# Optimization experiments

Hardware: AMD Instinct MI355X
Metric: run time of the kernel (lower is better)

## Reference

```python
import jax, jax.numpy as jnp
import numpy as np

N_HEAD = 16
HEAD_DIM = 64  # n_embd // n_head = 1024 // 16


def setup_inputs() -> dict:
    key = jax.random.key(0)
    k1, k2, k3 = jax.random.split(key, 3)
    B, T, C = 4, 2048, 1024
    x = jax.random.normal(k1, (B, T, C), dtype=jnp.float32)
    # torch Linear weight is (out, in); we store transposed (in, out) for x @ W
    w_qkv = jax.random.normal(k2, (C, 3 * C), dtype=jnp.float32) * (1.0 / np.sqrt(C))
    w_out = jax.random.normal(k3, (C, C), dtype=jnp.float32) * (1.0 / np.sqrt(C))
    return {"x": x, "w_qkv": w_qkv, "w_out": w_out}


def reference(x, w_qkv, w_out):
    B, T, C = x.shape
    scale = 1.0 / np.sqrt(HEAD_DIM).astype(np.float32)
    qkv = x @ w_qkv                                   # [B, T, 3C]
    q, k, v = jnp.split(qkv, 3, axis=2)
    def heads(t):  # [B, T, C] -> [B, H, T, Dh]
        return t.reshape(B, T, N_HEAD, HEAD_DIM).transpose(0, 2, 1, 3)
    q, k, v = heads(q), heads(k), heads(v)
    att = jnp.einsum('bhqd,bhkd->bhqk', q, k) * scale  # [B, H, T, T]
    causal = jnp.tril(jnp.ones((T, T), dtype=bool))
    att = jnp.where(causal[None, None], att, jnp.float32(-jnp.inf))
    att = jax.nn.softmax(att, axis=-1)
    y = jnp.einsum('bhqk,bhkd->bhqd', att, v)          # [B, H, T, Dh]
    y = y.transpose(0, 2, 1, 3).reshape(B, T, C)
    return y @ w_out
```

## Files before the change

### kernel.cpp

```cpp
#include <hip/hip_runtime.h>
#include <hip/hip_bf16.h>

#define B_ 4
#define T_ 2048
#define C_ 1024
#define H_ 16
#define D_ 64

typedef __bf16 bf16x8 __attribute__((ext_vector_type(8)));
typedef float f32x4 __attribute__((ext_vector_type(4)));
typedef float f32x16 __attribute__((ext_vector_type(16)));

__device__ __forceinline__ unsigned short f2bs(float f) {
    __hip_bfloat16 h = __float2bfloat16(f);
    return *reinterpret_cast<unsigned short*>(&h);
}

__device__ __forceinline__ float fexp2(float x) {
    float r;
    asm("v_exp_f32 %0, %1" : "=v"(r) : "v"(x));
    return r;
}

__device__ __forceinline__ unsigned cvtpk(float a, float b) {
    unsigned r;
    asm("v_cvt_pk_bf16_f32 %0, %1, %2" : "=v"(r) : "v"(a), "v"(b));
    return r;
}

__device__ __forceinline__ void plane32swap(unsigned& a, unsigned& b, int hi) {
#if __has_builtin(__builtin_amdgcn_permlane32_swap)
    typedef int i32x2 __attribute__((ext_vector_type(2)));
    i32x2 r = __builtin_amdgcn_permlane32_swap((int)a, (int)b, false, false);
    a = (unsigned)r.x; b = (unsigned)r.y;
#else
    unsigned v = hi ? a : b;
    unsigned e = __shfl_xor(v, 32);
    unsigned na = hi ? e : a;
    unsigned nb = hi ? b : e;
    a = na; b = nb;
#endif
}

__device__ __forceinline__ int swz(int row, int col) {
    return (row * 64 + col) ^ ((row & 7) << 3);
}

__device__ __forceinline__ void gload16(const void* g, void* l) {
    auto gp = (const __attribute__((address_space(1))) void*)(g);
    auto lp = (__attribute__((address_space(3))) void*)(uintptr_t)(l);
    __builtin_amdgcn_global_load_lds(gp, lp, 16, 0, 0);
}

__device__ __forceinline__ void phase_barrier() {
    __builtin_amdgcn_sched_barrier(0x77);
    __builtin_amdgcn_s_barrier();
}

__global__ __launch_bounds__(256)
void cvt_f32_to_bf16(const float* __restrict__ in, unsigned short* __restrict__ out, int n4) {
    int i = blockIdx.x * 256 + threadIdx.x;
    if (i >= n4) return;
    float4 v = ((const float4*)in)[i];
    union { unsigned short h[4]; uint2 u; } pk;
    pk.h[0] = f2bs(v.x); pk.h[1] = f2bs(v.y);
    pk.h[2] = f2bs(v.z); pk.h[3] = f2bs(v.w);
    ((uint2*)out)[i] = pk.u;
}

__global__ __launch_bounds__(256)
void transpose_weights(const float* __restrict__ in1, unsigned short* __restrict__ out1,
                       const float* __restrict__ in2, unsigned short* __restrict__ out2) {
    __shared__ float tile[64][65];
    const int tx = threadIdx.x & 63;
    const int ty = threadIdx.x >> 6;
    const bool second = blockIdx.x >= 48;
    const float* in = second ? in2 : in1;
    unsigned short* out = second ? out2 : out1;
    const int C = second ? 1024 : 3072;
    const int R = 1024;
    const int c0 = (second ? (blockIdx.x - 48) : blockIdx.x) * 64;
    const int r0 = blockIdx.y * 64;
    #pragma unroll
    for (int i = 0; i < 16; ++i) {
        int r = ty * 16 + i;
        tile[r][tx] = in[(size_t)(r0 + r) * C + c0 + tx];
    }
    __syncthreads();
    #pragma unroll
    for (int i = 0; i < 16; ++i) {
        int r = ty * 16 + i;
        out[(size_t)(c0 + r) * R + r0 + tx] = f2bs(tile[tx][r]);
    }
}

template<int MODE, int K>
__global__ __launch_bounds__(512, 2)
void gemm256(const unsigned short* __restrict__ A,
             const unsigned short* __restrict__ Bt,
             float* __restrict__ Out, int N_out,
             unsigned short* __restrict__ Qb,
             unsigned short* __restrict__ Kb,
             unsigned short* __restrict__ Vt) {
    __shared__ alignas(16) unsigned short L[2][4][128 * 64];
    const int tid = threadIdx.x;
    const int l = tid & 63;
    const int c16 = l & 15, lq = l >> 4;
    const int wv = tid >> 6;
    const int wm = wv >> 2;
    const int wn = wv & 3;
    const int m0 = blockIdx.x * 256, n0 = blockIdx.y * 256;
    constexpr int NT = K / 64;

    f32x4 acc[8][4];
    #pragma unroll
    for (int i = 0; i < 8; ++i)
        #pragma unroll
        for (int j = 0; j < 4; ++j)
            acc[i][j] = f32x4{0.f, 0.f, 0.f, 0.f};

    const int srow = tid >> 3;
    const int scs  = tid & 7;
    const int ldsbase = (tid & ~63) * 8;

    auto stage = [&](const unsigned short* M, int row0, int k0, unsigned short* dst) {
        #pragma unroll
        for (int r = 0; r < 2; ++r) {
            int row = r * 64 + srow;
            int csw = 8 * (scs ^ (row & 7));
            gload16(&M[(size_t)(row0 + row) * K + k0 + csw], &dst[r * 4096 + ldsbase]);
        }
    };

    stage(A,  m0,       0, L[0][0]);
    stage(A,  m0 + 128, 0, L[0][1]);
    stage(Bt, n0,       0, L[0][2]);
    stage(Bt, n0 + 128, 0, L[0][3]);
    if (NT > 1) stage(A, m0, 64, L[1][0]);

    bf16x8 af[4][2], bf[2][2], bg[2][2];
    const int brow0 = (wn & 1) * 64;

    for (int t = 0; t < NT; ++t) {
        const unsigned short* ap = L[t & 1][wm];
        const unsigned short* bp = L[t & 1][2 + (wn >> 1)];
        const int kn = (t + 1) * 64;

        if (t == NT - 1) asm volatile("s_waitcnt vmcnt(0)" ::: "memory");
        else             asm volatile("s_waitcnt vmcnt(2)" ::: "memory");
        #pragma unroll
        for (int mi = 0; mi < 4; ++mi)
            #pragma unroll
            for (int kk = 0; kk < 2; ++kk)
                af[mi][kk] = *(const bf16x8*)&ap[swz(mi * 16 + c16, kk * 32 + lq * 8)];
        #pragma unroll
        for (int ni = 0; ni < 2; ++ni)
            #pragma unroll
            for (int kk = 0; kk < 2; ++kk)
                bf[ni][kk] = *(const bf16x8*)&bp[swz(brow0 + ni * 16 + c16, kk * 32 + lq * 8)];
        if (t + 1 < NT) stage(A, m0 + 128, kn, L[(t + 1) & 1][1]);
        phase_barrier();
        __builtin_amdgcn_s_setprio(1);
        #pragma unroll
        for (int mi = 0; mi < 4; ++mi)
            #pragma unroll
            for (int ni = 0; ni < 2; ++ni)
                #pragma unroll
                for (int kk = 0; kk < 2; ++kk)
                    acc[mi][ni] = __builtin_amdgcn_mfma_f32_16x16x32_bf16(
                        af[mi][kk], bf[ni][kk], acc[mi][ni], 0, 0, 0);
        __builtin_amdgcn_s_setprio(0);
        phase_barrier();

        #pragma unroll
        for (int ni = 0; ni < 2; ++ni)
            #pragma unroll
            for (int kk = 0; kk < 2; ++kk)
                bg[ni][kk] = *(const bf16x8*)&bp[swz(brow0 + (ni + 2) * 16 + c16, kk * 32 + lq * 8)];
        if (t + 1 < NT) stage(Bt, n0, kn, L[(t + 1) & 1][2]);
        phase_barrier();
        __builtin_amdgcn_s_setprio(1);
        #pragma unroll
        for (int mi = 0; mi < 4; ++mi)
            #pragma unroll
            for (int ni = 0; ni < 2; ++ni)
                #pragma unroll
                for (int kk = 0; kk < 2; ++kk)
                    acc[mi][ni + 2] = __builtin_amdgcn_mfma_f32_16x16x32_bf16(
                        af[mi][kk], bg[ni][kk], acc[mi][ni + 2], 0, 0, 0);
        __builtin_amdgcn_s_setprio(0);
        phase_barrier();

        #pragma unroll
        for (int mi = 0; mi < 4; ++mi)
            #pragma unroll
            for (int kk = 0; kk < 2; ++kk)
                af[mi][kk] = *(const bf16x8*)&ap[swz((mi + 4) * 16 + c16, kk * 32 + lq * 8)];
        if (t + 1 < NT) stage(Bt, n0 + 128, kn, L[(t + 1) & 1][3]);
        phase_barrier();
        __builtin_amdgcn_s_setprio(1);
        #pragma unroll
        for (int mi = 0; mi < 4; ++mi)
            #pragma unroll
            for (int ni = 0; ni < 2; ++ni)
                #pragma unroll
                for (int kk = 0; kk < 2; ++kk)
                    acc[mi + 4][ni + 2] = __builtin_amdgcn_mfma_f32_16x16x32_bf16(
                        af[mi][kk], bg[ni][kk], acc[mi + 4][ni + 2], 0, 0, 0);
        __builtin_amdgcn_s_setprio(0);
        phase_barrier();

        if (t + 2 < NT) stage(A, m0, (t + 2) * 64, L[t & 1][0]);
        phase_barrier();
        __builtin_amdgcn_s_setprio(1);
        #pragma unroll
        for (int mi = 0; mi < 4; ++mi)
            #pragma unroll
            for (int ni = 0; ni < 2; ++ni)
                #pragma unroll
                for (int kk = 0; kk < 2; ++kk)
                    acc[mi + 4][ni] = __builtin_amdgcn_mfma_f32_16x16x32_bf16(
                        af[mi][kk], bf[ni][kk], acc[mi + 4][ni], 0, 0, 0);
        __builtin_amdgcn_s_setprio(0);
        phase_barrier();
    }

    #pragma unroll
    for (int mi = 0; mi < 8; ++mi) {
        #pragma unroll
        for (int ni = 0; ni < 4; ++ni) {
            #pragma unroll
            for (int r = 0; r < 4; ++r) {
                float v = acc[mi][ni][r];
                int row = m0 + wm * 128 + mi * 16 + lq * 4 + r;
                int col = n0 + wn * 64 + ni * 16 + c16;
                if (MODE == 1) {
                    Out[(size_t)row * N_out + col] = v;
                } else {
                    int which = col >> 10;
                    int c = col & 1023;
                    int h = c >> 6, d = c & 63;
                    int b = row >> 11, t = row & 2047;
                    int bh = b * H_ + h;
                    if (which == 0)
                        Qb[((size_t)(bh * T_ + t)) * D_ + d] = f2bs(v * 0.1803368801111204f);
                    else if (which == 1)
                        Kb[((size_t)(bh * T_ + t)) * D_ + d] = f2bs(v);
                    else
                        Vt[((size_t)(bh * D_ + d)) * T_ + t] = f2bs(v);
                }
            }
        }
    }
}

template<int MODE>
__global__ __launch_bounds__(256)
void gemm_bt(const unsigned short* __restrict__ A,
             const unsigned short* __restrict__ Bt,
             float* __restrict__ Out, int N_out,
             unsigned short* __restrict__ Qb,
             unsigned short* __restrict__ Kb,
             unsigned short* __restrict__ Vt,
             int K) {
    __shared__ alignas(16) unsigned short As[2][128 * 64];
    __shared__ alignas(16) unsigned short Bs[2][128 * 64];
    const int tid = threadIdx.x;
    const int l = tid & 63;
    const int c16 = l & 15, lq = l >> 4;
    const int wv = tid >> 6;
    const int wrow = wv >> 1, wcol = wv & 1;
    const int m0 = blockIdx.x * 128, n0 = blockIdx.y * 128;

    f32x4 acc[4][4];
    #pragma unroll
    for (int i = 0; i < 4; ++i)
        #pragma unroll
        for (int j = 0; j < 4; ++j)
            acc[i][j] = f32x4{0.f, 0.f, 0.f, 0.f};

    const int srow = tid >> 3;
    const int scs  = tid & 7;
    const int ldsbase = (tid & ~63) * 8;

    auto stage = [&](int k0, int buf) {
        #pragma unroll
        for (int p = 0; p < 4; ++p) {
            int row = p * 32 + srow;
            int csw = 8 * (scs ^ (row & 7));
            gload16(&A[(size_t)(m0 + row) * K + k0 + csw], &As[buf][p * 2048 + ldsbase]);
            gload16(&Bt[(size_t)(n0 + row) * K + k0 + csw], &Bs[buf][p * 2048 + ldsbase]);
        }
    };

    stage(0, 0);
    const int NK = K >> 6;
    for (int i = 0; i < NK; ++i) {
        __syncthreads();
        if (i + 1 < NK) stage((i + 1) << 6, (i + 1) & 1);
        const unsigned short* Al = As[i & 1];
        const unsigned short* Bl = Bs[i & 1];
        #pragma unroll
        for (int kk = 0; kk < 64; kk += 32) {
            bf16x8 af[4], bfv[4];
            int koff = kk + lq * 8;
            #pragma unroll
            for (int t = 0; t < 4; ++t) {
                af[t]  = *(const bf16x8*)&Al[swz(wrow * 64 + t * 16 + c16, koff)];
                bfv[t] = *(const bf16x8*)&Bl[swz(wcol * 64 + t * 16 + c16, koff)];
            }
            #pragma unroll
            for (int mi = 0; mi < 4; ++mi)
                #pragma unroll
                for (int ni = 0; ni < 4; ++ni)
                    acc[mi][ni] = __builtin_amdgcn_mfma_f32_16x16x32_bf16(
                        af[mi], bfv[ni], acc[mi][ni], 0, 0, 0);
        }
    }

    #pragma unroll
    for (int mi = 0; mi < 4; ++mi) {
        #pragma unroll
        for (int ni = 0; ni < 4; ++ni) {
            #pragma unroll
            for (int r = 0; r < 4; ++r) {
                float v = acc[mi][ni][r];
                int row = m0 + wrow * 64 + mi * 16 + lq * 4 + r;
                int col = n0 + wcol * 64 + ni * 16 + c16;
                if (MODE == 1) {
                    Out[(size_t)row * N_out + col] = v;
                } else {
                    int which = col >> 10;
                    int c = col & 1023;
                    int h = c >> 6, d = c & 63;
                    int b = row >> 11, t = row & 2047;
                    int bh = b * H_ + h;
                    if (which == 0)
                        Qb[((size_t)(bh * T_ + t)) * D_ + d] = f2bs(v * 0.1803368801111204f);
                    else if (which == 1)
                        Kb[((size_t)(bh * T_ + t)) * D_ + d] = f2bs(v);
                    else
                        Vt[((size_t)(bh * D_ + d)) * T_ + t] = f2bs(v);
                }
            }
        }
    }
}

__global__ __launch_bounds__(256, 2)
void attn_fwd(const unsigned short* __restrict__ Qb,
              const unsigned short* __restrict__ Kb,
              const unsigned short* __restrict__ Vt,
              unsigned short* __restrict__ Y) {
    __shared__ alignas(16) unsigned short Ks[2][64 * 64];
    __shared__ alignas(16) unsigned short Vs[2][64 * 64];
    const int tid = threadIdx.x;
    const int wv = tid >> 6;
    const int l = tid & 63;
    const int r32 = l & 31;
    const int hi = l >> 5;
    const int hi8 = hi * 8;
    const int bh = blockIdx.x & 63;
    const int qp = blockIdx.x >> 6;
    const unsigned short* Kp = Kb + (size_t)bh * T_ * D_;
    const unsigned short* Vp = Vt + (size_t)bh * D_ * T_;
    const unsigned short* Qbase = Qb + (size_t)bh * T_ * D_;
    const int b = bh >> 4, h = bh & 15;
    const int srow = tid >> 3;
    const int scs  = tid & 7;
    const int scol_sw = 8 * (scs ^ (srow & 7));
    const int wbase = wv * 512;

    #pragma unroll
    for (int half = 0; half < 2; ++half) {
        const int qc = (half == 0) ? qp : 15 - qp;
        const int q0w = qc * 128 + wv * 32;
        const int nt = 2 * qc + 2;
        const int qg = q0w + r32;

        bf16x8 qf[4];
        #pragma unroll
        for (int ds = 0; ds < 4; ++ds)
            qf[ds] = *(const bf16x8*)&Qbase[(size_t)qg * 64 + ds * 16 + hi8];

        f32x16 o[2];
        #pragma unroll
        for (int e = 0; e < 16; ++e) { o[0][e] = 0.f; o[1][e] = 0.f; }
        float lsum = 0.f;

        __syncthreads();
        gload16(&Kp[(size_t)srow * 64 + scol_sw],        &Ks[0][wbase]);
        gload16(&Kp[(size_t)(srow + 32) * 64 + scol_sw], &Ks[0][2048 + wbase]);
        gload16(&Vp[(size_t)srow * T_ + scol_sw],        &Vs[0][wbase]);
        gload16(&Vp[(size_t)(srow + 32) * T_ + scol_sw], &Vs[0][2048 + wbase]);

        for (int it = 0; it < nt; ++it) {
            const int kb = it * 64;
            __syncthreads();
            if (it + 1 < nt) {
                const int kn = kb + 64;
                unsigned short* Kd = Ks[(it + 1) & 1];
                unsigned short* Vd = Vs[(it + 1) & 1];
                gload16(&Kp[(size_t)(kn + srow) * 64 + scol_sw],        &Kd[wbase]);
                gload16(&Kp[(size_t)(kn + srow + 32) * 64 + scol_sw],   &Kd[2048 + wbase]);
                gload16(&Vp[(size_t)srow * T_ + kn + scol_sw],          &Vd[wbase]);
                gload16(&Vp[(size_t)(srow + 32) * T_ + kn + scol_sw],   &Vd[2048 + wbase]);
            }
            if (kb > q0w + 31) continue;
            const unsigned short* Kl = Ks[it & 1];
            const unsigned short* Vl = Vs[it & 1];

            f32x16 s[2];
            #pragma unroll
            for (int e = 0; e < 16; ++e) { s[0][e] = 0.f; s[1][e] = 0.f; }
            __builtin_amdgcn_s_setprio(1);
            #pragma unroll
            for (int kt = 0; kt < 2; ++kt)
                #pragma unroll
                for (int ds = 0; ds < 4; ++ds) {
                    bf16x8 af = *(const bf16x8*)&Kl[swz(32 * kt + r32, ds * 16 + hi8)];
                    s[kt] = __builtin_amdgcn_mfma_f32_32x32x16_bf16(af, qf[ds], s[kt], 0, 0, 0);
                }
            __builtin_amdgcn_s_setprio(0);
            if (kb + 63 > q0w) {
                #pragma unroll
                for (int kt = 0; kt < 2; ++kt)
                    #pragma unroll
                    for (int m = 0; m < 4; ++m)
                        #pragma unroll
                        for (int r = 0; r < 4; ++r)
                            if (kb + 32 * kt + 8 * m + r + 4 * hi > qg)
                                s[kt][4 * m + r] = -1e30f;
            }
            float rs0 = 0.f, rs1 = 0.f, rs2 = 0.f, rs3 = 0.f;
            #pragma unroll
            for (int kt = 0; kt < 2; ++kt)
                #pragma unroll
                for (int m = 0; m < 4; ++m) {
                    float p0 = fexp2(s[kt][4 * m + 0]);
                    float p1 = fexp2(s[kt][4 * m + 1]);
                    float p2 = fexp2(s[kt][4 * m + 2]);
                    float p3 = fexp2(s[kt][4 * m + 3]);
                    s[kt][4 * m + 0] = p0; s[kt][4 * m + 1] = p1;
                    s[kt][4 * m + 2] = p2; s[kt][4 * m + 3] = p3;
                    rs0 += p0; rs1 += p1; rs2 += p2; rs3 += p3;
                }
            lsum += (rs0 + rs1) + (rs2 + rs3);
            bf16x8 pb[4];
            #pragma unroll
            for (int ks = 0; ks < 4; ++ks) {
                const int kt = ks >> 1;
                const int m0 = (ks & 1) * 2;
                unsigned a0 = cvtpk(s[kt][4 * m0 + 0], s[kt][4 * m0 + 1]);
                unsigned a1 = cvtpk(s[kt][4 * m0 + 2], s[kt][4 * m0 + 3]);
                unsigned b0 = cvtpk(s[kt][4 * m0 + 4], s[kt][4 * m0 + 5]);
                unsigned b1 = cvtpk(s[kt][4 * m0 + 6], s[kt][4 * m0 + 7]);
                plane32swap(a0, b0, hi);
                plane32swap(a1, b1, hi);
                uint4 u = {a0, a1, b0, b1};
                pb[ks] = *reinterpret_cast<bf16x8*>(&u);
            }
            __builtin_amdgcn_s_setprio(1);
            #pragma unroll
            for (int dt = 0; dt < 2; ++dt)
                #pragma unroll
                for (int ks = 0; ks < 4; ++ks) {
                    bf16x8 va = *(const bf16x8*)&Vl[swz(32 * dt + r32, ks * 16 + hi8)];
                    o[dt] = __builtin_amdgcn_mfma_f32_32x32x16_bf16(va, pb[ks], o[dt], 0, 0, 0);
                }
            __builtin_amdgcn_s_setprio(0);
        }

        float lt = lsum + __shfl_xor(lsum, 32);
        float inv = 1.f / lt;
        #pragma unroll
        for (int dt = 0; dt < 2; ++dt)
            #pragma unroll
            for (int m = 0; m < 4; ++m) {
                uint2 w;
                w.x = cvtpk(o[dt][4 * m + 0] * inv, o[dt][4 * m + 1] * inv);
                w.y = cvtpk(o[dt][4 * m + 2] * inv, o[dt][4 * m + 3] * inv);
                int d = 32 * dt + 8 * m + 4 * hi;
                *(uint2*)&Y[((size_t)(b * T_ + qg)) * C_ + h * D_ + d] = w;
            }
    }
}

extern "C" void kernel_launch(void* const* d_in, const int* in_sizes, int n_in,
                              void* d_out, int out_size, void* d_ws, size_t ws_size,
                              hipStream_t stream) {
    const float* x     = (const float*)d_in[0];
    const float* w_qkv = (const float*)d_in[1];
    const float* w_out = (const float*)d_in[2];
    float* out = (float*)d_out;
    char* ws = (char*)d_ws;

    unsigned short* xb  = (unsigned short*)(ws);
    unsigned short* wqt = (unsigned short*)(ws + (16u << 20));
    unsigned short* wot = (unsigned short*)(ws + (22u << 20));
    unsigned short* Qb  = (unsigned short*)(ws + (24u << 20));
    unsigned short* Kb  = (unsigned short*)(ws + (40u << 20));
    unsigned short* Vt  = (unsigned short*)(ws + (56u << 20));
    unsigned short* Yb  = (unsigned short*)(ws + (72u << 20));

    cvt_f32_to_bf16<<<8192, 256, 0, stream>>>(x, xb, (B_ * T_ * C_) / 4);
    transpose_weights<<<dim3(64, 16), 256, 0, stream>>>(w_qkv, wqt, w_out, wot);
    gemm256<0, 1024><<<dim3(32, 12), 512, 0, stream>>>(xb, wqt, nullptr, 3072, Qb, Kb, Vt);
    attn_fwd<<<512, 256, 0, stream>>>(Qb, Kb, Vt, Yb);
    gemm_bt<1><<<dim3(64, 8), 256, 0, stream>>>(Yb, wot, out, 1024, nullptr, nullptr, nullptr, 1024);
}
```

Measured before the change: 177.6 us.

## Restructure 256x256 GEMM into quadrant-wise wave layout with staggered single-barrier stages

Remaps the 8 waves of the 256x256 GEMM block so each computes a 32x64 piece of each of four 128x128 quadrants, instead of a 128x64 strip. The main loop becomes four segments, each issuing one stage load for the next k-tile, waiting on vmcnt and crossing a single barrier before reusing loaded A/B fragments. This halves the barriers per k-step and interleaves prefetch with MFMA work more evenly. It uses more fragment registers and a looser sched_barrier mask, which risks register pressure or wrong waitcnt ordering.

Result: faster. 169.9 us (-4.3%).

```diff
diff --git a/kernel.cpp b/kernel.cpp
--- a/kernel.cpp
+++ b/kernel.cpp
@@ -52,9 +52,10 @@
     __builtin_amdgcn_global_load_lds(gp, lp, 16, 0, 0);
 }
 
-__device__ __forceinline__ void phase_barrier() {
-    __builtin_amdgcn_sched_barrier(0x77);
+__device__ __forceinline__ void seg_barrier() {
+    __builtin_amdgcn_sched_barrier(0x7);
     __builtin_amdgcn_s_barrier();
+    __builtin_amdgcn_sched_barrier(0x7);
 }
 
 __global__ __launch_bounds__(256)
@@ -107,17 +108,19 @@
     const int l = tid & 63;
     const int c16 = l & 15, lq = l >> 4;
     const int wv = tid >> 6;
-    const int wm = wv >> 2;
-    const int wn = wv & 3;
+    const int rw = wv & 3;
+    const int cw = wv >> 2;
     const int m0 = blockIdx.x * 256, n0 = blockIdx.y * 256;
     constexpr int NT = K / 64;
 
-    f32x4 acc[8][4];
-    #pragma unroll
-    for (int i = 0; i < 8; ++i)
-        #pragma unroll
-        for (int j = 0; j < 4; ++j)
-            acc[i][j] = f32x4{0.f, 0.f, 0.f, 0.f};
+    f32x4 acc[4][2][4];
+    #pragma unroll
+    for (int p = 0; p < 4; ++p)
+        #pragma unroll
+        for (int i = 0; i < 2; ++i)
+            #pragma unroll
+            for (int j = 0; j < 4; ++j)
+                acc[p][i][j] = f32x4{0.f, 0.f, 0.f, 0.f};
 
     const int srow = tid >> 3;
     const int scs  = tid & 7;
@@ -133,121 +136,127 @@
     };
 
     stage(A,  m0,       0, L[0][0]);
+    stage(Bt, n0,       0, L[0][2]);
     stage(A,  m0 + 128, 0, L[0][1]);
-    stage(Bt, n0,       0, L[0][2]);
     stage(Bt, n0 + 128, 0, L[0][3]);
-    if (NT > 1) stage(A, m0, 64, L[1][0]);
-
-    bf16x8 af[4][2], bf[2][2], bg[2][2];
-    const int brow0 = (wn & 1) * 64;
+
+    bf16x8 afA[2][2], afB[2][2], bfA[4][2], bfB[4][2];
 
     for (int t = 0; t < NT; ++t) {
-        const unsigned short* ap = L[t & 1][wm];
-        const unsigned short* bp = L[t & 1][2 + (wn >> 1)];
+        const int cur = t & 1, nb = (t + 1) & 1;
+        const unsigned short* A0 = L[cur][0];
+        const unsigned short* A1 = L[cur][1];
+        const unsigned short* B0 = L[cur][2];
+        const unsigned short* B1 = L[cur][3];
         const int kn = (t + 1) * 64;
-
-        if (t == NT - 1) asm volatile("s_waitcnt vmcnt(0)" ::: "memory");
-        else             asm volatile("s_waitcnt vmcnt(2)" ::: "memory");
-        #pragma unroll
-        for (int mi = 0; mi < 4; ++mi)
+        const bool st = (t + 1) < NT;
+
+        asm volatile("s_waitcnt vmcnt(4)" ::: "memory");
+        if (st) stage(A, m0, kn, L[nb][0]);
+        seg_barrier();
+        #pragma unroll
+        for (int mi = 0; mi < 2; ++mi)
             #pragma unroll
             for (int kk = 0; kk < 2; ++kk)
-                af[mi][kk] = *(const bf16x8*)&ap[swz(mi * 16 + c16, kk * 32 + lq * 8)];
-        #pragma unroll
-        for (int ni = 0; ni < 2; ++ni)
+                afA[mi][kk] = *(const bf16x8*)&A0[swz(rw * 32 + mi * 16 + c16, kk * 32 + lq * 8)];
+        #pragma unroll
+        for (int ni = 0; ni < 4; ++ni)
             #pragma unroll
             for (int kk = 0; kk < 2; ++kk)
-                bf[ni][kk] = *(const bf16x8*)&bp[swz(brow0 + ni * 16 + c16, kk * 32 + lq * 8)];
-        if (t + 1 < NT) stage(A, m0 + 128, kn, L[(t + 1) & 1][1]);
-        phase_barrier();
+                bfA[ni][kk] = *(const bf16x8*)&B0[swz(cw * 64 + ni * 16 + c16, kk * 32 + lq * 8)];
         __builtin_amdgcn_s_setprio(1);
         #pragma unroll
-        for (int mi = 0; mi < 4; ++mi)
-            #pragma unroll
-            for (int ni = 0; ni < 2; ++ni)
+        for (int mi = 0; mi < 2; ++mi)
+            #pragma unroll
+            for (int ni = 0; ni < 4; ++ni)
                 #pragma unroll
                 for (int kk = 0; kk < 2; ++kk)
-                    acc[mi][ni] = __builtin_amdgcn_mfma_f32_16x16x32_bf16(
-                        af[mi][kk], bf[ni][kk], acc[mi][ni], 0, 0, 0);
+                    acc[0][mi][ni] = __builtin_amdgcn_mfma_f32_16x16x32_bf16(
+                        afA[mi][kk], bfA[ni][kk], acc[0][mi][ni], 0, 0, 0);
         __builtin_amdgcn_s_setprio(0);
-        phase_barrier();
-
-        #pragma unroll
-        for (int ni = 0; ni < 2; ++ni)
+
+        if (st) asm volatile("s_waitcnt vmcnt(4)" ::: "memory");
+        else    asm volatile("s_waitcnt vmcnt(2)" ::: "memory");
+        if (st) stage(Bt, n0, kn, L[nb][2]);
+        seg_barrier();
+        #pragma unroll
+        for (int mi = 0; mi < 2; ++mi)
             #pragma unroll
             for (int kk = 0; kk < 2; ++kk)
-                bg[ni][kk] = *(const bf16x8*)&bp[swz(brow0 + (ni + 2) * 16 + c16, kk * 32 + lq * 8)];
-        if (t + 1 < NT) stage(Bt, n0, kn, L[(t + 1) & 1][2]);
-        phase_barrier();
+                afB[mi][kk] = *(const bf16x8*)&A1[swz(rw * 32 + mi * 16 + c16, kk * 32 + lq * 8)];
         __builtin_amdgcn_s_setprio(1);
         #pragma unroll
-        for (int mi = 0; mi < 4; ++mi)
-            #pragma unroll
-            for (int ni = 0; ni < 2; ++ni)
+        for (int mi = 0; mi < 2; ++mi)
+            #pragma unroll
+            for (int ni = 0; ni < 4; ++ni)
                 #pragma unroll
                 for (int kk = 0; kk < 2; ++kk)
-                    acc[mi][ni + 2] = __builtin_amdgcn_mfma_f32_16x16x32_bf16(
-                        af[mi][kk], bg[ni][kk], acc[mi][ni + 2], 0, 0, 0);
+                    acc[1][mi][ni] = __builtin_amdgcn_mfma_f32_16x16x32_bf16(
+                        afB[mi][kk], bfA[ni][kk], acc[1][mi][ni], 0, 0, 0);
         __builtin_amdgcn_s_setprio(0);
-        phase_barrier();
-
-        #pragma unroll
-        for (int mi = 0; mi < 4; ++mi)
+
+        if (st) asm volatile("s_waitcnt vmcnt(4)" ::: "memory");
+        else    asm volatile("s_waitcnt vmcnt(0)" ::: "memory");
+        if (st) stage(A, m0 + 128, kn, L[nb][1]);
+        seg_barrier();
+        #pragma unroll
+        for (int ni = 0; ni < 4; ++ni)
             #pragma unroll
             for (int kk = 0; kk < 2; ++kk)
-                af[mi][kk] = *(const bf16x8*)&ap[swz((mi + 4) * 16 + c16, kk * 32 + lq * 8)];
-        if (t + 1 < NT) stage(Bt, n0 + 128, kn, L[(t + 1) & 1][3]);
-        phase_barrier();
+                bfB[ni][kk] = *(const bf16x8*)&B1[swz(cw * 64 + ni * 16 + c16, kk * 32 + lq * 8)];
         __builtin_amdgcn_s_setprio(1);
         #pragma unroll
-        for (int mi = 0; mi < 4; ++mi)
-            #pragma unroll
-            for (int ni = 0; ni < 2; ++ni)
+        for (int mi = 0; mi < 2; ++mi)
+            #pragma unroll
+            for (int ni = 0; ni < 4; ++ni)
                 #pragma unroll
                 for (int kk = 0; kk < 2; ++kk)
-                    acc[mi + 4][ni + 2] = __builtin_amdgcn_mfma_f32_16x16x32_bf16(
-                        af[mi][kk], bg[ni][kk], acc[mi + 4][ni + 2], 0, 0, 0);
+                    acc[2][mi][ni] = __builtin_amdgcn_mfma_f32_16x16x32_bf16(
+                        afB[mi][kk], bfB[ni][kk], acc[2][mi][ni], 0, 0, 0);
         __builtin_amdgcn_s_setprio(0);
-        phase_barrier();
-
-        if (t + 2 < NT) stage(A, m0, (t + 2) * 64, L[t & 1][0]);
-        phase_barrier();
+
+        if (st) stage(Bt, n0 + 128, kn, L[nb][3]);
+        seg_barrier();
         __builtin_amdgcn_s_setprio(1);
         #pragma unroll
-        for (int mi = 0; mi < 4; ++mi)
-            #pragma unroll
-            for (int ni = 0; ni < 2; ++ni)
+        for (int mi = 0; mi < 2; ++mi)
+            #pragma unroll
+            for (int ni = 0; ni < 4; ++ni)
                 #pragma unroll
                 for (int kk = 0; kk < 2; ++kk)
-                    acc[mi + 4][ni] = __builtin_amdgcn_mfma_f32_16x16x32_bf16(
-                        af[mi][kk], bf[ni][kk], acc[mi + 4][ni], 0, 0, 0);
+                    acc[3][mi][ni] = __builtin_amdgcn_mfma_f32_16x16x32_bf16(
+                        afA[mi][kk], bfB[ni][kk], acc[3][mi][ni], 0, 0, 0);
         __builtin_amdgcn_s_setprio(0);
-        phase_barrier();
-    }
-
-    #pragma unroll
-    for (int mi = 0; mi < 8; ++mi) {
-        #pragma unroll
-        for (int ni = 0; ni < 4; ++ni) {
-            #pragma unroll
-            for (int r = 0; r < 4; ++r) {
-                float v = acc[mi][ni][r];
-                int row = m0 + wm * 128 + mi * 16 + lq * 4 + r;
-                int col = n0 + wn * 64 + ni * 16 + c16;
-                if (MODE == 1) {
-                    Out[(size_t)row * N_out + col] = v;
-                } else {
-                    int which = col >> 10;
-                    int c = col & 1023;
-                    int h = c >> 6, d = c & 63;
-                    int b = row >> 11, t = row & 2047;
-                    int bh = b * H_ + h;
-                    if (which == 0)
-                        Qb[((size_t)(bh * T_ + t)) * D_ + d] = f2bs(v * 0.1803368801111204f);
-                    else if (which == 1)
-                        Kb[((size_t)(bh * T_ + t)) * D_ + d] = f2bs(v);
-                    else
-                        Vt[((size_t)(bh * D_ + d)) * T_ + t] = f2bs(v);
+    }
+
+    #pragma unroll
+    for (int p = 0; p < 4; ++p) {
+        const int qa = (p == 1 || p == 2) ? 1 : 0;
+        const int qb = (p >= 2) ? 1 : 0;
+        #pragma unroll
+        for (int mi = 0; mi < 2; ++mi) {
+            #pragma unroll
+            for (int ni = 0; ni < 4; ++ni) {
+                #pragma unroll
+                for (int r = 0; r < 4; ++r) {
+                    float v = acc[p][mi][ni][r];
+                    int row = m0 + qa * 128 + rw * 32 + mi * 16 + lq * 4 + r;
+                    int col = n0 + qb * 128 + cw * 64 + ni * 16 + c16;
+                    if (MODE == 1) {
+                        Out[(size_t)row * N_out + col] = v;
+                    } else {
+                        int which = col >> 10;
+                        int c = col & 1023;
+                        int h = c >> 6, d = c & 63;
+                        int b = row >> 11, tt = row & 2047;
+                        int bh = b * H_ + h;
+                        if (which == 0)
+                            Qb[((size_t)(bh * T_ + tt)) * D_ + d] = f2bs(v * 0.1803368801111204f);
+                        else if (which == 1)
+                            Kb[((size_t)(bh * T_ + tt)) * D_ + d] = f2bs(v);
+                        else
+                            Vt[((size_t)(bh * D_ + d)) * T_ + tt] = f2bs(v);
+                    }
                 }
             }
         }
```
